# Kernel tuning notes

Hardware: AMD Instinct MI355X
Metric: run time of the kernel (lower is better)

## Reference

```python
import jax, jax.numpy as jnp
import numpy as np

KSIZE = 11
SIGMA = 1.5
CHANNELS = 1


def _gaussian_kernel(size=KSIZE, sigma=SIGMA, channels=CHANNELS):
    coords = jnp.arange(size, dtype=jnp.float32) - size // 2
    g = jnp.exp(-coords ** 2 / (2.0 * sigma ** 2))
    g = g / g.sum()
    k2d = jnp.outer(g, g)  # [k, k]
    # depthwise kernel, OIHW with I=1 per group
    return jnp.broadcast_to(k2d, (channels, 1, size, size))


def _dwconv(x, k):
    pad = KSIZE // 2
    return jax.lax.conv_general_dilated(
        x, k, window_strides=(1, 1), padding=[(pad, pad), (pad, pad)],
        dimension_numbers=('NCHW', 'OIHW', 'NCHW'),
        feature_group_count=CHANNELS)


def setup_inputs() -> dict:
    key = jax.random.key(0)
    k1, k2 = jax.random.split(key)
    x_hat = jax.random.normal(k1, (64, 1, 512, 512), dtype=jnp.float32)
    x = jax.random.normal(k2, (64, 1, 512, 512), dtype=jnp.float32)
    kernel = _gaussian_kernel()
    return {"x_hat": x_hat, "x": x, "kernel": kernel}


def reference(x_hat, x, kernel):
    C1, C2 = 0.01 ** 2, 0.03 ** 2
    # shift [-1,1] -> [0,1]
    a = (x + 1.0) / 2.0          # 'x' in _ssim
    b = (x_hat + 1.0) / 2.0      # 'y' in _ssim
    mu_x = _dwconv(a, kernel)
    mu_y = _dwconv(b, kernel)
    mu_x2 = mu_x ** 2
    mu_y2 = mu_y ** 2
    mu_xy = mu_x * mu_y
    sig_x = _dwconv(a * a, kernel) - mu_x2
    sig_y = _dwconv(b * b, kernel) - mu_y2
    sig_xy = _dwconv(a * b, kernel) - mu_xy
    num = (2.0 * mu_xy + C1) * (2.0 * sig_xy + C2)
    den = (mu_x2 + mu_y2 + C1) * (sig_x + sig_y + C2)
    ssim = (num / (den + 1e-08)).mean()
    return 1.0 - ssim
```

## Files before the change

### kernel.cpp

```cpp
#include <hip/hip_runtime.h>

#define IMG_W 512
#define IMG_H 512
#define RH    64
#define KS    11
#define KR    5
#define OFF   8
#define LROW  (OFF + IMG_W + OFF)
#define CH    KS
#define NROWS (RH + 2*KR)
#define NCH   7

__global__ __launch_bounds__(256, 2)
void ssim_main(const float* __restrict__ xhat,
               const float* __restrict__ x,
               const float* __restrict__ kern,
               float* __restrict__ accum)
{
    __shared__ float rowA[CH][LROW];
    __shared__ float rowB[CH][LROW];
    __shared__ float red[4];

    const int tid   = threadIdx.x;
    const int c0    = tid << 1;
    const int img   = blockIdx.x >> 3;
    const int strip = blockIdx.x & 7;
    const int R0    = strip * RH;
    const float* xp = x    + (size_t)img * (IMG_W * IMG_H);
    const float* hp = xhat + (size_t)img * (IMG_W * IMG_H);

    float g[KS];
    {
        const float inv = rsqrtf(kern[5 * KS + 5]);
        #pragma unroll
        for (int i = 0; i < KS; ++i) g[i] = kern[5 * KS + i] * inv;
    }

    {
        float* fa = &rowA[0][0];
        float* fb = &rowB[0][0];
        for (int i = tid; i < CH * LROW; i += 256) { fa[i] = 0.f; fb[i] = 0.f; }
    }

    const bool isB = (tid >= 128);
    const float* sp = isB ? hp : xp;
    float* dstBase  = isB ? &rowB[0][0] : &rowA[0][0];
    const int c4    = (tid & 127) << 2;

    float hist[5][KS][2];
    float acc = 0.f;
    const float C1 = 1e-4f, C2 = 9e-4f;

    #pragma unroll 1
    for (int chk = 0; chk < NCH; ++chk) {
        __syncthreads();

        #pragma unroll
        for (int j = 0; j < CH; ++j) {
            const int ri = R0 - KR + chk * CH + j;
            float4 s = make_float4(0.f, 0.f, 0.f, 0.f);
            if (ri >= 0 && ri < IMG_H) {
                const float4 v = *(const float4*)(sp + (size_t)ri * IMG_W + c4);
                s.x = fmaf(v.x, 0.5f, 0.5f);
                s.y = fmaf(v.y, 0.5f, 0.5f);
                s.z = fmaf(v.z, 0.5f, 0.5f);
                s.w = fmaf(v.w, 0.5f, 0.5f);
            }
            *(float4*)(dstBase + j * LROW + OFF + c4) = s;
        }
        __syncthreads();

        #pragma unroll
        for (int p = 0; p < CH; ++p) {
            const int rr = chk * CH + p;
            if (rr < NROWS) {
                const int ib = OFF + c0 - 6;
                float wa[14], wb[14];
                #pragma unroll
                for (int m = 0; m < 7; ++m) {
                    const float2 ta = *(const float2*)&rowA[p][ib + 2 * m];
                    const float2 tb = *(const float2*)&rowB[p][ib + 2 * m];
                    wa[2 * m] = ta.x; wa[2 * m + 1] = ta.y;
                    wb[2 * m] = tb.x; wb[2 * m + 1] = tb.y;
                }

                float h[5][2];
                #pragma unroll
                for (int f = 0; f < 5; ++f) { h[f][0] = 0.f; h[f][1] = 0.f; }
                #pragma unroll
                for (int i = 0; i < KS + 1; ++i) {
                    const float pa  = wa[i + 1];
                    const float pb  = wb[i + 1];
                    const float paa = pa * pa;
                    const float pbb = pb * pb;
                    const float pab = pa * pb;
                    if (i < KS) {
                        const float w = g[i];
                        h[0][0] = fmaf(w, pa,  h[0][0]);
                        h[1][0] = fmaf(w, pb,  h[1][0]);
                        h[2][0] = fmaf(w, paa, h[2][0]);
                        h[3][0] = fmaf(w, pbb, h[3][0]);
                        h[4][0] = fmaf(w, pab, h[4][0]);
                    }
                    if (i > 0) {
                        const float w = g[i - 1];
                        h[0][1] = fmaf(w, pa,  h[0][1]);
                        h[1][1] = fmaf(w, pb,  h[1][1]);
                        h[2][1] = fmaf(w, paa, h[2][1]);
                        h[3][1] = fmaf(w, pbb, h[3][1]);
                        h[4][1] = fmaf(w, pab, h[4][1]);
                    }
                }
                #pragma unroll
                for (int f = 0; f < 5; ++f) {
                    hist[f][p][0] = h[f][0];
                    hist[f][p][1] = h[f][1];
                }

                if (rr >= 2 * KR) {
                    float v[5][2];
                    #pragma unroll
                    for (int f = 0; f < 5; ++f) { v[f][0] = 0.f; v[f][1] = 0.f; }
                    #pragma unroll
                    for (int t = 0; t < KS; ++t) {
                        const int slot = (p + 1 + t) % KS;
                        const float w = g[t];
                        #pragma unroll
                        for (int f = 0; f < 5; ++f) {
                            v[f][0] = fmaf(w, hist[f][slot][0], v[f][0]);
                            v[f][1] = fmaf(w, hist[f][slot][1], v[f][1]);
                        }
                    }
                    #pragma unroll
                    for (int col = 0; col < 2; ++col) {
                        const float mux  = v[0][col], muy = v[1][col];
                        const float mux2 = mux * mux;
                        const float muy2 = muy * muy;
                        const float muxy = mux * muy;
                        const float sx   = v[2][col] - mux2;
                        const float sy   = v[3][col] - muy2;
                        const float sxy  = v[4][col] - muxy;
                        const float num  = (2.f * muxy + C1) * (2.f * sxy + C2);
                        const float den  = (mux2 + muy2 + C1) * (sx + sy + C2);
                        acc = fmaf(num, __builtin_amdgcn_rcpf(den + 1e-8f), acc);
                    }
                }
            }
        }
    }

    #pragma unroll
    for (int o = 32; o > 0; o >>= 1) acc += __shfl_down(acc, o, 64);
    if ((tid & 63) == 0) red[tid >> 6] = acc;
    __syncthreads();
    if (tid == 0) atomicAdd(accum, red[0] + red[1] + red[2] + red[3]);
}

__global__ void ssim_final(const float* __restrict__ accum,
                           float* __restrict__ out)
{
    out[0] = 1.0f - accum[0] * (1.0f / (64.0f * 512.0f * 512.0f));
}

extern "C" void kernel_launch(void* const* d_in, const int* in_sizes, int n_in,
                              void* d_out, int out_size, void* d_ws, size_t ws_size,
                              hipStream_t stream) {
    const float* xhat = (const float*)d_in[0];
    const float* xin  = (const float*)d_in[1];
    const float* kern = (const float*)d_in[2];
    float* out = (float*)d_out;
    float* ws  = (float*)d_ws;

    const int nimg   = in_sizes[0] / (IMG_W * IMG_H);
    const int strips = IMG_H / RH;
    const int nblk   = nimg * strips;

    hipMemsetAsync(ws, 0, sizeof(float), stream);
    ssim_main<<<nblk, 256, 0, stream>>>(xhat, xin, kern, ws);
    ssim_final<<<1, 1, 0, stream>>>(ws, out);
}
```

Baseline: 215.6 us.

## Use one column per thread, direct global-to-LDS loads, and fold shift algebraically

The block grows from 256 to 512 threads, and each thread now owns one output column instead of two. This cuts the per-thread history registers in half so more waves can be resident. Row loads into LDS now use the global_load_lds intrinsic, which writes straight to shared memory without passing through registers. The (x+1)/2 shift is no longer applied at load time; it is folded into the final SSIM expression through rearranged FMA algebra. In exchange, the horizontal pass no longer shares a window between neighbouring columns, and correctness depends on the async LDS writes being complete by the barrier.

```diff
diff --git a/kernel.cpp b/kernel.cpp
--- a/kernel.cpp
+++ b/kernel.cpp
@@ -1,4 +1,5 @@
 #include <hip/hip_runtime.h>
+#include <stdint.h>
 
 #define IMG_W 512
 #define IMG_H 512
@@ -11,7 +12,7 @@
 #define NROWS (RH + 2*KR)
 #define NCH   7
 
-__global__ __launch_bounds__(256, 2)
+__global__ __launch_bounds__(512, 4)
 void ssim_main(const float* __restrict__ xhat,
                const float* __restrict__ x,
                const float* __restrict__ kern,
@@ -19,10 +20,12 @@
 {
     __shared__ float rowA[CH][LROW];
     __shared__ float rowB[CH][LROW];
-    __shared__ float red[4];
+    __shared__ float red[8];
 
     const int tid   = threadIdx.x;
-    const int c0    = tid << 1;
+    const int lane  = tid & 63;
+    const int wid   = tid >> 6;
+    const int c     = tid;
     const int img   = blockIdx.x >> 3;
     const int strip = blockIdx.x & 7;
     const int R0    = strip * RH;
@@ -37,17 +40,16 @@
     }
 
     {
-        float* fa = &rowA[0][0];
-        float* fb = &rowB[0][0];
-        for (int i = tid; i < CH * LROW; i += 256) { fa[i] = 0.f; fb[i] = 0.f; }
+        float4* a4 = (float4*)&rowA[0][0];
+        float4* b4 = (float4*)&rowB[0][0];
+        #pragma unroll 1
+        for (int i = tid; i < (CH * LROW) / 4; i += 512) {
+            a4[i] = make_float4(0.f, 0.f, 0.f, 0.f);
+            b4[i] = make_float4(0.f, 0.f, 0.f, 0.f);
+        }
     }
 
-    const bool isB = (tid >= 128);
-    const float* sp = isB ? hp : xp;
-    float* dstBase  = isB ? &rowB[0][0] : &rowA[0][0];
-    const int c4    = (tid & 127) << 2;
-
-    float hist[5][KS][2];
+    float hist[5][KS];
     float acc = 0.f;
     const float C1 = 1e-4f, C2 = 9e-4f;
 
@@ -56,17 +58,30 @@
         __syncthreads();
 
         #pragma unroll
-        for (int j = 0; j < CH; ++j) {
-            const int ri = R0 - KR + chk * CH + j;
-            float4 s = make_float4(0.f, 0.f, 0.f, 0.f);
-            if (ri >= 0 && ri < IMG_H) {
-                const float4 v = *(const float4*)(sp + (size_t)ri * IMG_W + c4);
-                s.x = fmaf(v.x, 0.5f, 0.5f);
-                s.y = fmaf(v.y, 0.5f, 0.5f);
-                s.z = fmaf(v.z, 0.5f, 0.5f);
-                s.w = fmaf(v.w, 0.5f, 0.5f);
+        for (int k = 0; k < 6; ++k) {
+            const int q = wid + 8 * k;
+            if (q < 4 * CH) {
+                const int j  = q >> 2;
+                const int rr = chk * CH + j;
+                if (rr < NROWS) {
+                    const int f  = (q >> 1) & 1;
+                    const int h  = q & 1;
+                    const int ri = R0 - KR + rr;
+                    float* ldsbase = f ? &rowB[j][OFF + h * 256]
+                                       : &rowA[j][OFF + h * 256];
+                    if (ri >= 0 && ri < IMG_H) {
+                        const float* gsrc = (f ? hp : xp)
+                            + (size_t)ri * IMG_W + h * 256 + lane * 4;
+                        __builtin_amdgcn_global_load_lds(
+                            (const __attribute__((address_space(1))) void*)gsrc,
+                            (__attribute__((address_space(3))) void*)ldsbase,
+                            16, 0, 0);
+                    } else {
+                        *(float4*)(ldsbase + lane * 4) =
+                            make_float4(0.f, 0.f, 0.f, 0.f);
+                    }
+                }
             }
-            *(float4*)(dstBase + j * LROW + OFF + c4) = s;
         }
         __syncthreads();
 
@@ -74,76 +89,52 @@
         for (int p = 0; p < CH; ++p) {
             const int rr = chk * CH + p;
             if (rr < NROWS) {
-                const int ib = OFF + c0 - 6;
-                float wa[14], wb[14];
+                const int ib = OFF + c - 6;
+                float wa[12], wb[12];
                 #pragma unroll
-                for (int m = 0; m < 7; ++m) {
+                for (int m = 0; m < 6; ++m) {
                     const float2 ta = *(const float2*)&rowA[p][ib + 2 * m];
                     const float2 tb = *(const float2*)&rowB[p][ib + 2 * m];
                     wa[2 * m] = ta.x; wa[2 * m + 1] = ta.y;
                     wb[2 * m] = tb.x; wb[2 * m + 1] = tb.y;
                 }
 
-                float h[5][2];
+                float h0 = 0.f, h1 = 0.f, h2 = 0.f, h3 = 0.f, h4 = 0.f;
                 #pragma unroll
-                for (int f = 0; f < 5; ++f) { h[f][0] = 0.f; h[f][1] = 0.f; }
-                #pragma unroll
-                for (int i = 0; i < KS + 1; ++i) {
-                    const float pa  = wa[i + 1];
-                    const float pb  = wb[i + 1];
-                    const float paa = pa * pa;
-                    const float pbb = pb * pb;
-                    const float pab = pa * pb;
-                    if (i < KS) {
-                        const float w = g[i];
-                        h[0][0] = fmaf(w, pa,  h[0][0]);
-                        h[1][0] = fmaf(w, pb,  h[1][0]);
-                        h[2][0] = fmaf(w, paa, h[2][0]);
-                        h[3][0] = fmaf(w, pbb, h[3][0]);
-                        h[4][0] = fmaf(w, pab, h[4][0]);
-                    }
-                    if (i > 0) {
-                        const float w = g[i - 1];
-                        h[0][1] = fmaf(w, pa,  h[0][1]);
-                        h[1][1] = fmaf(w, pb,  h[1][1]);
-                        h[2][1] = fmaf(w, paa, h[2][1]);
-                        h[3][1] = fmaf(w, pbb, h[3][1]);
-                        h[4][1] = fmaf(w, pab, h[4][1]);
-                    }
+                for (int t = 0; t < KS; ++t) {
+                    const float w  = g[t];
+                    const float pa = wa[t + 1];
+                    const float pb = wb[t + 1];
+                    h0 = fmaf(w, pa,      h0);
+                    h1 = fmaf(w, pb,      h1);
+                    h2 = fmaf(w, pa * pa, h2);
+                    h3 = fmaf(w, pb * pb, h3);
+                    h4 = fmaf(w, pa * pb, h4);
                 }
-                #pragma unroll
-                for (int f = 0; f < 5; ++f) {
-                    hist[f][p][0] = h[f][0];
-                    hist[f][p][1] = h[f][1];
-                }
+                hist[0][p] = h0; hist[1][p] = h1; hist[2][p] = h2;
+                hist[3][p] = h3; hist[4][p] = h4;
 
                 if (rr >= 2 * KR) {
-                    float v[5][2];
-                    #pragma unroll
-                    for (int f = 0; f < 5; ++f) { v[f][0] = 0.f; v[f][1] = 0.f; }
+                    float U = 0.f, V = 0.f, U2 = 0.f, V2 = 0.f, UVc = 0.f;
                     #pragma unroll
                     for (int t = 0; t < KS; ++t) {
                         const int slot = (p + 1 + t) % KS;
                         const float w = g[t];
-                        #pragma unroll
-                        for (int f = 0; f < 5; ++f) {
-                            v[f][0] = fmaf(w, hist[f][slot][0], v[f][0]);
-                            v[f][1] = fmaf(w, hist[f][slot][1], v[f][1]);
-                        }
+                        U   = fmaf(w, hist[0][slot], U);
+                        V   = fmaf(w, hist[1][slot], V);
+                        U2  = fmaf(w, hist[2][slot], U2);
+                        V2  = fmaf(w, hist[3][slot], V2);
+                        UVc = fmaf(w, hist[4][slot], UVc);
                     }
-                    #pragma unroll
-                    for (int col = 0; col < 2; ++col) {
-                        const float mux  = v[0][col], muy = v[1][col];
-                        const float mux2 = mux * mux;
-                        const float muy2 = muy * muy;
-                        const float muxy = mux * muy;
-                        const float sx   = v[2][col] - mux2;
-                        const float sy   = v[3][col] - muy2;
-                        const float sxy  = v[4][col] - muxy;
-                        const float num  = (2.f * muxy + C1) * (2.f * sxy + C2);
-                        const float den  = (mux2 + muy2 + C1) * (sx + sy + C2);
-                        acc = fmaf(num, __builtin_amdgcn_rcpf(den + 1e-8f), acc);
-                    }
+                    const float pU = U + 1.f, pV = V + 1.f;
+                    const float t1 = fmaf(0.5f,  pU * pV,            C1);
+                    const float t2 = fmaf(0.5f,  fmaf(-U, V, UVc),   C2);
+                    const float t3 = fmaf(0.25f, fmaf(pU, pU, pV*pV), C1);
+                    const float e  = fmaf(-U, U, U2) + fmaf(-V, V, V2);
+                    const float t4 = fmaf(0.25f, e,                  C2);
+                    acc = fmaf(t1 * t2,
+                               __builtin_amdgcn_rcpf(fmaf(t3, t4, 1e-8f)),
+                               acc);
                 }
             }
         }
@@ -151,9 +142,14 @@
 
     #pragma unroll
     for (int o = 32; o > 0; o >>= 1) acc += __shfl_down(acc, o, 64);
-    if ((tid & 63) == 0) red[tid >> 6] = acc;
+    if (lane == 0) red[wid] = acc;
     __syncthreads();
-    if (tid == 0) atomicAdd(accum, red[0] + red[1] + red[2] + red[3]);
+    if (tid == 0) {
+        float s = 0.f;
+        #pragma unroll
+        for (int w = 0; w < 8; ++w) s += red[w];
+        atomicAdd(accum, s);
+    }
 }
 
 __global__ void ssim_final(const float* __restrict__ accum,
@@ -176,6 +172,6 @@
     const int nblk   = nimg * strips;
 
     hipMemsetAsync(ws, 0, sizeof(float), stream);
-    ssim_main<<<nblk, 256, 0, stream>>>(xhat, xin, kern, ws);
+    ssim_main<<<nblk, 512, 0, stream>>>(xhat, xin, kern, ws);
     ssim_final<<<1, 1, 0, stream>>>(ws, out);
 }
```

Result: no change. 213.0 us (-1.2%).
